# Performance work log

Measured on AMD Instinct MI355X. Metric: run time of the kernel, lower is better.

Reference implementation:

```python
import jax, jax.numpy as jnp
import numpy as np
import math

B, SEQ, PRED, F, DM, NH, DFF, S, DMARK = 16, 336, 96, 7, 512, 8, 2048, 16, 5
EL, DL = 2, 1
DH = DM // NH


def _pe(max_len, d):
    pos = np.arange(max_len)[:, None].astype(np.float32)
    div = np.exp(np.arange(0, d, 2).astype(np.float32) * (-math.log(10000.0) / d))
    pe = np.zeros((max_len, d), np.float32)
    pe[:, 0::2] = np.sin(pos * div)
    pe[:, 1::2] = np.cos(pos * div)
    return jnp.asarray(pe)


def _make_tao():
    t = np.ones((S, S), np.float32)
    t[:, 0] = 0.0
    t[:, -1] = 0.0
    t[1] *= -1.0
    t[0] = 0.0
    t[0, 0] = 1.0
    t[2:, 1:-1] = np.eye(S - 2, dtype=np.float32)
    return jnp.asarray(t)


PE = _pe(2000, DM)
TAO = _make_tao()
ZVEC = jnp.zeros((S,), jnp.float32).at[:2].set(1.0)
MASK = jnp.triu(jnp.full((PRED, PRED), -1e9, jnp.float32), k=1)  # causal additive mask


def _ln(x, w, b, eps=1e-5):
    m = x.mean(-1, keepdims=True)
    v = ((x - m) ** 2).mean(-1, keepdims=True)
    return (x - m) * jax.lax.rsqrt(v + eps) * w + b


def _mha(q_in, kv_in, qkv_w, qkv_b, ow, ob, mask=None):
    wq, wk, wv = jnp.split(qkv_w, 3, axis=0)
    bq, bk, bv = jnp.split(qkv_b, 3, axis=0)

    def proj(x, w, bb):
        y = x @ w.T + bb  # [B, T, DM]
        return y.reshape(y.shape[0], y.shape[1], NH, DH).transpose(0, 2, 1, 3)

    q, k, v = proj(q_in, wq, bq), proj(kv_in, wk, bk), proj(kv_in, wv, bv)
    s = jnp.einsum('bhqd,bhkd->bhqk', q, k) / math.sqrt(DH)
    if mask is not None:
        s = s + mask
    a = jax.nn.softmax(s, axis=-1)
    o = jnp.einsum('bhqk,bhkd->bhqd', a, v)
    o = o.transpose(0, 2, 1, 3).reshape(q_in.shape)
    return o @ ow.T + ob


def _per_feature(xe, xd, eqw, eqb, eow, eob, el1w, el1b, el2w, el2b,
                 ef1w, ef1b, ef2w, ef2b, elw, elb,
                 dsqw, dsqb, dsow, dsob, dcqw, dcqb, dcow, dcob,
                 dl1w, dl1b, dl2w, dl2b, dl3w, dl3b, df1w, df1b, df2w, df2b):
    # post-norm TransformerEncoder (relu FFN), eval mode (no dropout)
    h = xe
    for l in range(EL):
        h = _ln(h + _mha(h, h, eqw[l], eqb[l], eow[l], eob[l]), el1w[l], el1b[l])
        ff = jax.nn.relu(h @ ef1w[l].T + ef1b[l]) @ ef2w[l].T + ef2b[l]
        h = _ln(h + ff, el2w[l], el2b[l])
    # encoder_linear maps time axis seqlen -> prelen
    mem = jnp.einsum('bsd,ps->bpd', h, elw) + elb[None, :, None]
    t = xd
    for l in range(DL):
        t = _ln(t + _mha(t, t, dsqw[l], dsqb[l], dsow[l], dsob[l], MASK), dl1w[l], dl1b[l])
        t = _ln(t + _mha(t, mem, dcqw[l], dcqb[l], dcow[l], dcob[l]), dl2w[l], dl2b[l])
        ff = jax.nn.relu(t @ df1w[l].T + df1b[l]) @ df2w[l].T + df2b[l]
        t = _ln(t + ff, dl3w[l], dl3b[l])
    return t


_vfeat = jax.vmap(_per_feature, in_axes=(1, 1) + (0,) * 32, out_axes=1)


def setup_inputs():
    key = jax.random.key(0)
    ks = iter(jax.random.split(key, 64))

    def rn(shape, s=0.05):
        return jax.random.normal(next(ks), shape, jnp.float32) * s

    return {
        'batch_x': rn((B, SEQ, F), 1.0),
        'batch_x_mark': rn((B, SEQ, DMARK - 1), 1.0),
        'batch_y': rn((B, PRED, F), 1.0),
        'batch_y_mark': rn((B, PRED, DMARK - 1), 1.0),
        'w_in': rn((DM, DMARK)), 'b_in': rn((DM,)),
        'w_co': rn((DM, DMARK - 1)), 'b_co': rn((DM,)),
        'eqw': rn((F, EL, 3 * DM, DM)), 'eqb': rn((F, EL, 3 * DM)),
        'eow': rn((F, EL, DM, DM)), 'eob': rn((F, EL, DM)),
        'el1w': jnp.ones((F, EL, DM)), 'el1b': jnp.zeros((F, EL, DM)),
        'el2w': jnp.ones((F, EL, DM)), 'el2b': jnp.zeros((F, EL, DM)),
        'ef1w': rn((F, EL, DFF, DM)), 'ef1b': rn((F, EL, DFF)),
        'ef2w': rn((F, EL, DM, DFF)), 'ef2b': rn((F, EL, DM)),
        'elw': rn((F, PRED, SEQ)), 'elb': rn((F, PRED)),
        'dsqw': rn((F, DL, 3 * DM, DM)), 'dsqb': rn((F, DL, 3 * DM)),
        'dsow': rn((F, DL, DM, DM)), 'dsob': rn((F, DL, DM)),
        'dcqw': rn((F, DL, 3 * DM, DM)), 'dcqb': rn((F, DL, 3 * DM)),
        'dcow': rn((F, DL, DM, DM)), 'dcob': rn((F, DL, DM)),
        'dl1w': jnp.ones((F, DL, DM)), 'dl1b': jnp.zeros((F, DL, DM)),
        'dl2w': jnp.ones((F, DL, DM)), 'dl2b': jnp.zeros((F, DL, DM)),
        'dl3w': jnp.ones((F, DL, DM)), 'dl3b': jnp.zeros((F, DL, DM)),
        'df1w': rn((F, DL, DFF, DM)), 'df1b': rn((F, DL, DFF)),
        'df2w': rn((F, DL, DM, DFF)), 'df2b': rn((F, DL, DM)),
        'wc': rn((S, DM)), 'bc': rn((S,)),
        'ws': rn((1, DM)), 'bs': rn((1,)),
    }


def reference(batch_x, batch_x_mark, batch_y, batch_y_mark,
              w_in, b_in, w_co, b_co,
              eqw, eqb, eow, eob, el1w, el1b, el2w, el2b,
              ef1w, ef1b, ef2w, ef2b, elw, elb,
              dsqw, dsqb, dsow, dsob, dcqw, dcqb, dcow, dcob,
              dl1w, dl1b, dl2w, dl2b, dl3w, dl3b, df1w, df1b, df2w, df2b,
              wc, bc, ws, bs):
    Bsz = batch_x.shape[0]
    # time marks are shared across features -> broadcast instead of concat loop
    hist = jnp.concatenate(
        [batch_x[..., None],
         jnp.broadcast_to(batch_x_mark[:, :, None, :], (Bsz, SEQ, F, DMARK - 1))], axis=-1)
    fut = jnp.broadcast_to(batch_y_mark[:, -PRED:, None, :], (Bsz, PRED, F, DMARK - 1))
    hist = hist.transpose(0, 2, 1, 3)  # [B, F, SEQ, DMARK]
    fut = fut.transpose(0, 2, 1, 3)    # [B, F, PRED, DMARK-1]
    xe = hist @ w_in.T + b_in + PE[:SEQ]
    xd = fut @ w_co.T + b_co + PE[:PRED]
    dec = _vfeat(xe, xd, eqw, eqb, eow, eob, el1w, el1b, el2w, el2b,
                 ef1w, ef1b, ef2w, ef2b, elw, elb,
                 dsqw, dsqb, dsow, dsob, dcqw, dcqb, dcow, dcob,
                 dl1w, dl1b, dl2w, dl2b, dl3w, dl3b, df1w, df1b, df2w, df2b)
    # g_c = Linear + Hardsigmoid; g_s = Linear + Softplus
    c = jnp.clip((jnp.einsum('bfpd,sd->bfps', dec, wc) + bc) / 6.0 + 0.5, 0.0, 1.0)
    sig = jax.nn.softplus(jnp.einsum('bfpd,d->bfp', dec, ws[0]) + bs[0])
    # linear state recurrence a = TAO @ a + c, y = z^T a, scanned over prediction days
    a0 = c[:, :, 0]                      # [B, F, S] (torch initializes a with day-0 g_c)
    cs = jnp.moveaxis(c, 2, 0)           # [PRED, B, F, S]
    ss = jnp.moveaxis(sig, 2, 0)         # [PRED, B, F]

    def step(a, xs):
        cd, sd = xs
        a = jnp.einsum('ij,bfj->bfi', TAO, a) + cd
        return a, jnp.einsum('s,bfs->bf', ZVEC, a) + sd

    _, ys = jax.lax.scan(step, a0, (cs, ss))
    return jnp.transpose(ys, (1, 0, 2))  # [B, PRED, F]
```

## Files before the change

kernel.cpp:

```cpp
#include <hip/hip_runtime.h>

typedef unsigned short u16;
typedef unsigned int   u32;
typedef __attribute__((ext_vector_type(8))) short short8;
typedef __attribute__((ext_vector_type(4))) float f32x4;

#define DEV static __device__ __forceinline__

DEV float bf2f(u16 u) { return __uint_as_float(((u32)u) << 16); }
DEV u16 f2bf(float f) {
  u32 u = __float_as_uint(f);
  return (u16)((u + 0x7fffu + ((u >> 16) & 1u)) >> 16);
}

#define GLD16(gp, lp) __builtin_amdgcn_global_load_lds( \
    (__attribute__((address_space(1))) u32*)(gp),       \
    (__attribute__((address_space(3))) u32*)(lp), 16, 0, 0)

#define SBAR()  asm volatile("s_barrier" ::: "memory")
#define LGKM0() asm volatile("s_waitcnt lgkmcnt(0)" ::: "memory")

__global__ __launch_bounds__(512, 2) void gemm_bf16(
    const u16* __restrict__ A, const u16* __restrict__ Bw, u16* __restrict__ C,
    const float* __restrict__ bias, int M, int N, int K,
    long sAz, long sBz, long sCz, long sBiasZ, int relu)
{
  __shared__ __align__(16) u16 Asm[2][2][8192];
  __shared__ __align__(16) u16 Bsm[2][2][8192];

  int gx = (int)gridDim.x, gy = (int)gridDim.y;
  int nwg = gx * gy * (int)gridDim.z;
  int orig = (int)blockIdx.x + gx * ((int)blockIdx.y + gy * (int)blockIdx.z);
  int qq = nwg >> 3, rr_ = nwg & 7;
  int xcd = orig & 7, pos = orig >> 3;
  int lg_id = (xcd < rr_) ? (xcd * (qq + 1) + pos) : (rr_ * (qq + 1) + (xcd - rr_) * qq + pos);
  int bz = lg_id / (gx * gy);
  int rem = lg_id - bz * (gx * gy);
  int by = rem / gx, bx = rem - by * gx;

  A += (size_t)bz * sAz; Bw += (size_t)bz * sBz; C += (size_t)bz * sCz; bias += (size_t)bz * sBiasZ;
  int tileM = bx * 256, tileN = by * 256;
  int tid = threadIdx.x, wave = tid >> 6, lane = tid & 63;
  int lr = lane & 15, lgp = lane >> 4;
  int wm = (wave >> 2) * 128;
  int wn = (wave & 3) * 64;
  int ah = wave >> 2;
  int bh = (wave & 3) >> 1;
  int bnb = ((wave & 3) & 1) * 64;

  const int NT = K >> 6;
  const u16* Abase = A + (size_t)tileM * K;
  const u16* Bbase = Bw + (size_t)tileN * K;

  auto SA = [&](int b, int h, int t) {
    const u16* src = Abase + (size_t)h * 128 * K + t * 64;
    #pragma unroll
    for (int i = 0; i < 2; i++) {
      int gi = i * 512 + tid;
      int row = gi >> 3, g = gi & 7;
      GLD16(src + (size_t)row * K + ((g ^ (row & 7)) * 8), Asm[b][h] + (size_t)gi * 8);
    }
  };
  auto SB = [&](int b, int h, int t) {
    const u16* src = Bbase + (size_t)h * 128 * K + t * 64;
    #pragma unroll
    for (int i = 0; i < 2; i++) {
      int gi = i * 512 + tid;
      int row = gi >> 3, g = gi & 7;
      GLD16(src + (size_t)row * K + ((g ^ (row & 7)) * 8), Bsm[b][h] + (size_t)gi * 8);
    }
  };

  f32x4 acc[8][4] = {};

  SA(0, 0, 0); SA(0, 1, 0); SB(0, 0, 0); SB(0, 1, 0);
  if (NT > 1) { SB(1, 0, 1); SB(1, 1, 1); }
  if (NT > 1) asm volatile("s_waitcnt vmcnt(4)" ::: "memory");
  else        asm volatile("s_waitcnt vmcnt(0)" ::: "memory");
  SBAR();

  for (int t = 0; t < NT; ++t) {
    int cur = t & 1;
    const u16* Aslot = Asm[cur][ah];
    const u16* Bslot = Bsm[cur][bh];
    short8 afr[8], b0[4], b1[4];

    #pragma unroll
    for (int mm = 0; mm < 4; ++mm) {
      int rw = mm * 16 + lr;
      #pragma unroll
      for (int ks = 0; ks < 2; ++ks)
        afr[mm * 2 + ks] = *(const short8*)(Aslot + rw * 64 + (((ks * 4 + lgp) ^ (rw & 7)) * 8));
    }
    #pragma unroll
    for (int nn = 0; nn < 2; ++nn) {
      int rw = bnb + nn * 16 + lr;
      #pragma unroll
      for (int ks = 0; ks < 2; ++ks)
        b0[nn * 2 + ks] = *(const short8*)(Bslot + rw * 64 + (((ks * 4 + lgp) ^ (rw & 7)) * 8));
    }
    if (t + 1 < NT) SA(cur ^ 1, 0, t + 1);
    SBAR(); LGKM0();
    __builtin_amdgcn_s_setprio(1);
    #pragma unroll
    for (int mm = 0; mm < 4; ++mm)
      #pragma unroll
      for (int nn = 0; nn < 2; ++nn)
        #pragma unroll
        for (int ks = 0; ks < 2; ++ks)
          acc[mm][nn] = __builtin_amdgcn_mfma_f32_16x16x32_bf16(
              afr[mm * 2 + ks], b0[nn * 2 + ks], acc[mm][nn], 0, 0, 0);
    __builtin_amdgcn_s_setprio(0);
    SBAR();

    #pragma unroll
    for (int nn = 0; nn < 2; ++nn) {
      int rw = bnb + (nn + 2) * 16 + lr;
      #pragma unroll
      for (int ks = 0; ks < 2; ++ks)
        b1[nn * 2 + ks] = *(const short8*)(Bslot + rw * 64 + (((ks * 4 + lgp) ^ (rw & 7)) * 8));
    }
    if (t + 1 < NT) SA(cur ^ 1, 1, t + 1);
    SBAR(); LGKM0();
    __builtin_amdgcn_s_setprio(1);
    #pragma unroll
    for (int mm = 0; mm < 4; ++mm)
      #pragma unroll
      for (int nn = 0; nn < 2; ++nn)
        #pragma unroll
        for (int ks = 0; ks < 2; ++ks)
          acc[mm][nn + 2] = __builtin_amdgcn_mfma_f32_16x16x32_bf16(
              afr[mm * 2 + ks], b1[nn * 2 + ks], acc[mm][nn + 2], 0, 0, 0);
    __builtin_amdgcn_s_setprio(0);
    SBAR();

    #pragma unroll
    for (int mm = 0; mm < 4; ++mm) {
      int rw = (mm + 4) * 16 + lr;
      #pragma unroll
      for (int ks = 0; ks < 2; ++ks)
        afr[mm * 2 + ks] = *(const short8*)(Aslot + rw * 64 + (((ks * 4 + lgp) ^ (rw & 7)) * 8));
    }
    if (t + 2 < NT) SB(cur, 0, t + 2);
    SBAR(); LGKM0();
    __builtin_amdgcn_s_setprio(1);
    #pragma unroll
    for (int mm = 0; mm < 4; ++mm)
      #pragma unroll
      for (int nn = 0; nn < 2; ++nn)
        #pragma unroll
        for (int ks = 0; ks < 2; ++ks)
          acc[mm + 4][nn + 2] = __builtin_amdgcn_mfma_f32_16x16x32_bf16(
              afr[mm * 2 + ks], b1[nn * 2 + ks], acc[mm + 4][nn + 2], 0, 0, 0);
    __builtin_amdgcn_s_setprio(0);
    SBAR();

    if (t + 2 < NT) SB(cur, 1, t + 2);
    __builtin_amdgcn_s_setprio(1);
    #pragma unroll
    for (int mm = 0; mm < 4; ++mm)
      #pragma unroll
      for (int nn = 0; nn < 2; ++nn)
        #pragma unroll
        for (int ks = 0; ks < 2; ++ks)
          acc[mm + 4][nn] = __builtin_amdgcn_mfma_f32_16x16x32_bf16(
              afr[mm * 2 + ks], b0[nn * 2 + ks], acc[mm + 4][nn], 0, 0, 0);
    __builtin_amdgcn_s_setprio(0);
    if (t + 2 < NT) asm volatile("s_waitcnt vmcnt(4)" ::: "memory");
    else            asm volatile("s_waitcnt vmcnt(0)" ::: "memory");
    SBAR();
  }

  float bb[4];
  #pragma unroll
  for (int n = 0; n < 4; ++n) bb[n] = bias[tileN + wn + n * 16 + lr];
  #pragma unroll
  for (int m = 0; m < 8; ++m) {
    #pragma unroll
    for (int rr = 0; rr < 4; ++rr) {
      int mrow = tileM + wm + m * 16 + lgp * 4 + rr;
      u16* crow = C + (size_t)mrow * N + tileN + wn + lr;
      #pragma unroll
      for (int n = 0; n < 4; ++n) {
        float v = acc[m][n][rr] + bb[n];
        if (relu) v = fmaxf(v, 0.f);
        crow[n * 16] = f2bf(v);
      }
    }
  }
}

__global__ __launch_bounds__(256, 2) void gemm_bf16_s(
    const u16* __restrict__ A, const u16* __restrict__ Bw, u16* __restrict__ C,
    const float* __restrict__ bias, int M, int N, int K,
    long sAz, long sBz, long sCz, long sBiasZ, int relu)
{
  __shared__ __align__(16) u16 Asm[3][128 * 32];
  __shared__ __align__(16) u16 Bsm[3][128 * 32];

  int gx = (int)gridDim.x, gy = (int)gridDim.y;
  int nwg = gx * gy * (int)gridDim.z;
  int orig = (int)blockIdx.x + gx * ((int)blockIdx.y + gy * (int)blockIdx.z);
  int qq = nwg >> 3, rr_ = nwg & 7;
  int xcd = orig & 7, pos = orig >> 3;
  int lg_id = (xcd < rr_) ? (xcd * (qq + 1) + pos) : (rr_ * (qq + 1) + (xcd - rr_) * qq + pos);
  int bz = lg_id / (gx * gy);
  int rem = lg_id - bz * (gx * gy);
  int by = rem / gx, bx = rem - by * gx;

  A += (size_t)bz * sAz; Bw += (size_t)bz * sBz; C += (size_t)bz * sCz; bias += (size_t)bz * sBiasZ;
  int tileM = bx * 128, tileN = by * 128;
  int tid = threadIdx.x, lane = tid & 63;
  int wave = tid >> 6;
  int lr = lane & 15, lgp = lane >> 4;
  int wm = (wave >> 1) * 64, wn = (wave & 1) * 64;

  const int NT = K >> 5;
  const u16* Abase = A + (size_t)tileM * K;
  const u16* Bbase = Bw + (size_t)tileN * K;

  auto STAGE = [&](int b, int t) {
    int kb = t * 32;
    #pragma unroll
    for (int i = 0; i < 2; i++) {
      int gi = i * 256 + tid;
      int row = gi >> 2, g = gi & 3;
      GLD16(Abase + (size_t)row * K + kb + ((g ^ ((row >> 1) & 3)) * 8),
            Asm[b] + (size_t)gi * 8);
    }
    #pragma unroll
    for (int i = 0; i < 2; i++) {
      int gi = i * 256 + tid;
      int row = gi >> 2, g = gi & 3;
      GLD16(Bbase + (size_t)row * K + kb + ((g ^ ((row >> 1) & 3)) * 8),
            Bsm[b] + (size_t)gi * 8);
    }
  };

  f32x4 acc[4][4] = {};

  STAGE(0, 0);
  if (NT > 1) STAGE(1, 1);

  int cur = 0;
  for (int t = 0; t < NT; ++t) {
    if (t + 2 < NT) {
      int nb = cur + 2; if (nb >= 3) nb -= 3;
      STAGE(nb, t + 2);
      asm volatile("s_waitcnt vmcnt(8)" ::: "memory");
    } else if (t + 1 < NT) {
      asm volatile("s_waitcnt vmcnt(4)" ::: "memory");
    } else {
      asm volatile("s_waitcnt vmcnt(0)" ::: "memory");
    }
    SBAR();

    const u16* Ab = Asm[cur];
    const u16* Bb = Bsm[cur];
    short8 afr[4], bfr[4];
    #pragma unroll
    for (int m = 0; m < 4; ++m) {
      int rw = wm + m * 16 + lr;
      afr[m] = *(const short8*)(Ab + rw * 32 + ((lgp ^ ((rw >> 1) & 3)) * 8));
    }
    #pragma unroll
    for (int n = 0; n < 4; ++n) {
      int rw = wn + n * 16 + lr;
      bfr[n] = *(const short8*)(Bb + rw * 32 + ((lgp ^ ((rw >> 1) & 3)) * 8));
    }
    __builtin_amdgcn_s_setprio(1);
    #pragma unroll
    for (int m = 0; m < 4; ++m)
      #pragma unroll
      for (int n = 0; n < 4; ++n)
        acc[m][n] = __builtin_amdgcn_mfma_f32_16x16x32_bf16(
            afr[m], bfr[n], acc[m][n], 0, 0, 0);
    __builtin_amdgcn_s_setprio(0);
    LGKM0();
    SBAR();
    cur = (cur + 1 == 3) ? 0 : cur + 1;
  }

  float bb[4];
  #pragma unroll
  for (int n = 0; n < 4; ++n) bb[n] = bias[tileN + wn + n * 16 + lr];
  #pragma unroll
  for (int m = 0; m < 4; ++m) {
    #pragma unroll
    for (int rr = 0; rr < 4; ++rr) {
      int mrow = tileM + wm + m * 16 + lgp * 4 + rr;
      u16* crow = C + (size_t)mrow * N + tileN + wn + lr;
      #pragma unroll
      for (int n = 0; n < 4; ++n) {
        float v = acc[m][n][rr] + bb[n];
        if (relu) v = fmaxf(v, 0.f);
        crow[n * 16] = f2bf(v);
      }
    }
  }
}

__global__ void cvt_w_kernel(const float* __restrict__ src, u16* __restrict__ dst,
                             long n_per_f, long f_stride, long total4)
{
  long i = (long)blockIdx.x * blockDim.x + threadIdx.x;
  long step = (long)gridDim.x * blockDim.x;
  for (; i < total4; i += step) {
    long e = i * 4;
    long f = e / n_per_f; long r = e - f * n_per_f;
    float4 v = *(const float4*)(src + f * f_stride + r);
    *(ushort4*)(dst + e) = make_ushort4(f2bf(v.x), f2bf(v.y), f2bf(v.z), f2bf(v.w));
  }
}

__global__ __launch_bounds__(128) void embed_enc_k(
    const float* __restrict__ x, const float* __restrict__ mark,
    const float* __restrict__ w_in, const float* __restrict__ b_in,
    u16* __restrict__ hb)
{
  int row = blockIdx.x;
  int f = row / 5376; int rem = row - f * 5376; int b = rem / 336; int s = rem - b * 336;
  int bsix = b * 336 + s;
  float v0 = x[(size_t)bsix * 7 + f];
  float m0 = mark[(size_t)bsix * 4 + 0], m1 = mark[(size_t)bsix * 4 + 1];
  float m2 = mark[(size_t)bsix * 4 + 2], m3 = mark[(size_t)bsix * 4 + 3];
  int d0 = threadIdx.x * 4;
  u16 ob[4];
  #pragma unroll
  for (int c = 0; c < 4; c++) {
    int d = d0 + c;
    const float* w = w_in + d * 5;
    float val = w[0] * v0 + w[1] * m0 + w[2] * m1 + w[3] * m2 + w[4] * m3 + b_in[d];
    int i = d >> 1;
    float dv = expf((float)i * -0.0359778920778f);
    float arg = (float)s * dv;
    val += (d & 1) ? cosf(arg) : sinf(arg);
    ob[c] = f2bf(val);
  }
  *(ushort4*)(hb + (size_t)row * 512 + d0) = make_ushort4(ob[0], ob[1], ob[2], ob[3]);
}

__global__ __launch_bounds__(128) void embed_dec_k(
    const float* __restrict__ ymark, const float* __restrict__ w_co,
    const float* __restrict__ b_co, u16* __restrict__ tb)
{
  int row = blockIdx.x;
  int f = row / 1536; int rem = row - f * 1536; int b = rem / 96; int pp = rem - b * 96;
  int bp = b * 96 + pp;
  float m0 = ymark[(size_t)bp * 4 + 0], m1 = ymark[(size_t)bp * 4 + 1];
  float m2 = ymark[(size_t)bp * 4 + 2], m3 = ymark[(size_t)bp * 4 + 3];
  int d0 = threadIdx.x * 4;
  u16 ob[4];
  #pragma unroll
  for (int c = 0; c < 4; c++) {
    int d = d0 + c;
    const float* w = w_co + d * 4;
    float val = w[0] * m0 + w[1] * m1 + w[2] * m2 + w[3] * m3 + b_co[d];
    int i = d >> 1;
    float dv = expf((float)i * -0.0359778920778f);
    float arg = (float)pp * dv;
    val += (d & 1) ? cosf(arg) : sinf(arg);
    ob[c] = f2bf(val);
  }
  *(ushort4*)(tb + (size_t)row * 512 + d0) = make_ushort4(ob[0], ob[1], ob[2], ob[3]);
}

template<int LK, int CHUNK, int NQI>
__global__ __launch_bounds__(256) void attn_mfma(
    const u16* __restrict__ q, const u16* __restrict__ k, const u16* __restrict__ v,
    u16* __restrict__ out, int Lq, int qstride, int kvstride, int causal, int qspan)
{
  constexpr int NCH = LK / CHUNK;
  constexpr int NKT = CHUNK / 16;
  constexpr int NKS = (CHUNK + 31) / 32;
  constexpr int KPAD = NKS * 32;
  constexpr int VSTR = KPAD + 8;
  constexpr int NGRP = CHUNK * 8 / 64;

  __shared__ __align__(16) u16 KsS[CHUNK * 64];
  __shared__ __align__(16) u16 VtS[64 * VSTR];
  __shared__ __align__(16) u16 PWS[4][16 * VSTR];

  int hh = blockIdx.x, fb = blockIdx.y;
  int tid = threadIdx.x, wave = tid >> 6, lane = tid & 63;
  int lr = lane & 15, lg = lane >> 4;

  const int nqt = Lq / 16;
  const int qlo = (int)blockIdx.z * qspan;
  const int qhi = (qlo + qspan < nqt) ? (qlo + qspan) : nqt;

  const u16* qp = q + (size_t)fb * Lq * qstride + hh * 64;
  const u16* kp = k + (size_t)fb * LK * kvstride + hh * 64;
  const u16* vp = v + (size_t)fb * LK * kvstride + hh * 64;

  if constexpr (KPAD > CHUNK) {
    constexpr int TW = KPAD - CHUNK;
    for (int i = tid; i < 64 * TW; i += 256)
      VtS[(i / TW) * VSTR + CHUNK + (i % TW)] = 0;
    u16* PW = PWS[wave];
    for (int i = lane; i < 16 * TW; i += 64)
      PW[(i / TW) * VSTR + CHUNK + (i % TW)] = 0;
  }

  f32x4 oacc[NQI][4] = {};
  f32x4 lsum[NQI] = {};
  u16* PW = PWS[wave];

  for (int c = 0; c < NCH; ++c) {
    __syncthreads();

    const u16* kcp = kp + (size_t)c * CHUNK * kvstride;
    for (int grp = wave; grp < NGRP; grp += 4) {
      int gi = grp * 64 + lane;
      int row = gi >> 3, g = gi & 7;
      GLD16(kcp + (size_t)row * kvstride + ((g ^ (row & 7)) * 8), KsS + (size_t)gi * 8);
    }
    const u16* vcp = vp + (size_t)c * CHUNK * kvstride;
    for (int idx = tid; idx < CHUNK * 8; idx += 256) {
      int kk = idx >> 3, dg = idx & 7;
      uint4 pv = *(const uint4*)(vcp + (size_t)kk * kvstride + dg * 8);
      u16* col = VtS + (size_t)(dg * 8) * VSTR + kk;
      col[0 * VSTR] = (u16)pv.x; col[1 * VSTR] = (u16)(pv.x >> 16);
      col[2 * VSTR] = (u16)pv.y; col[3 * VSTR] = (u16)(pv.y >> 16);
      col[4 * VSTR] = (u16)pv.z; col[5 * VSTR] = (u16)(pv.z >> 16);
      col[6 * VSTR] = (u16)pv.w; col[7 * VSTR] = (u16)(pv.w >> 16);
    }
    __syncthreads();

    #pragma unroll
    for (int qi = 0; qi < NQI; ++qi) {
      int qt = qlo + wave + qi * 4;
      if (qt < qhi) {
        const u16* qrow = qp + (size_t)(qt * 16 + lr) * qstride + lg * 8;
        short8 qf0 = *(const short8*)(qrow);
        short8 qf1 = *(const short8*)(qrow + 32);

        f32x4 sacc[NKT];
        #pragma unroll
        for (int t = 0; t < NKT; t++) {
          int row = t * 16 + lr;
          const u16* kb = KsS + row * 64;
          short8 kf0 = *(const short8*)(kb + ((lg ^ (row & 7)) * 8));
          short8 kf1 = *(const short8*)(kb + (((lg + 4) ^ (row & 7)) * 8));
          f32x4 s = {0.f, 0.f, 0.f, 0.f};
          s = __builtin_amdgcn_mfma_f32_16x16x32_bf16(qf0, kf0, s, 0, 0, 0);
          s = __builtin_amdgcn_mfma_f32_16x16x32_bf16(qf1, kf1, s, 0, 0, 0);
          sacc[t] = s;
        }

        #pragma unroll
        for (int t = 0; t < NKT; t++) {
          int kg = c * CHUNK + t * 16 + lr;
          #pragma unroll
          for (int r = 0; r < 4; r++) {
            int qg = qt * 16 + lg * 4 + r;
            float p = (causal && kg > qg) ? 0.f : __expf(sacc[t][r] * 0.125f);
            sacc[t][r] = p;
            lsum[qi][r] += p;
          }
          u16* pw = PW + (size_t)(lg * 4) * VSTR + t * 16 + lr;
          pw[0 * VSTR] = f2bf(sacc[t][0]);
          pw[1 * VSTR] = f2bf(sacc[t][1]);
          pw[2 * VSTR] = f2bf(sacc[t][2]);
          pw[3 * VSTR] = f2bf(sacc[t][3]);
        }

        #pragma unroll
        for (int s = 0; s < NKS; s++) {
          short8 pf = *(const short8*)(PW + (size_t)lr * VSTR + s * 32 + lg * 8);
          #pragma unroll
          for (int j = 0; j < 4; j++) {
            short8 vf = *(const short8*)(VtS + (size_t)(j * 16 + lr) * VSTR + s * 32 + lg * 8);
            oacc[qi][j] = __builtin_amdgcn_mfma_f32_16x16x32_bf16(pf, vf, oacc[qi][j], 0, 0, 0);
          }
        }
      }
    }
  }

  #pragma unroll
  for (int qi = 0; qi < NQI; ++qi) {
    int qt = qlo + wave + qi * 4;
    if (qt < qhi) {
      float l0 = lsum[qi][0], l1 = lsum[qi][1], l2 = lsum[qi][2], l3 = lsum[qi][3];
      #pragma unroll
      for (int m = 1; m < 16; m <<= 1) {
        l0 += __shfl_xor(l0, m);
        l1 += __shfl_xor(l1, m);
        l2 += __shfl_xor(l2, m);
        l3 += __shfl_xor(l3, m);
      }
      float inv[4] = {1.f / l0, 1.f / l1, 1.f / l2, 1.f / l3};
      #pragma unroll
      for (int r = 0; r < 4; r++) {
        size_t orow = (size_t)fb * Lq + qt * 16 + lg * 4 + r;
        u16* ob = out + orow * 512 + hh * 64 + lr;
        #pragma unroll
        for (int j = 0; j < 4; j++)
          ob[j * 16] = f2bf(oacc[qi][j][r] * inv[r]);
      }
    }
  }
}

__global__ __launch_bounds__(128) void ln_kernel(
    u16* __restrict__ h, const u16* __restrict__ delta,
    const float* __restrict__ gamma, const float* __restrict__ beta,
    int rows_per_f, long gstride)
{
  __shared__ float red[2];
  int row = blockIdx.x;
  int f = row / rows_per_f;
  const float* g = gamma + (size_t)f * gstride;
  const float* be = beta + (size_t)f * gstride;
  int d0 = threadIdx.x * 4;
  size_t p = (size_t)row * 512 + d0;
  ushort4 hv = *(const ushort4*)(h + p);
  ushort4 dv = *(const ushort4*)(delta + p);
  float x0 = bf2f(hv.x) + bf2f(dv.x), x1 = bf2f(hv.y) + bf2f(dv.y);
  float x2 = bf2f(hv.z) + bf2f(dv.z), x3 = bf2f(hv.w) + bf2f(dv.w);
  float ssum = x0 + x1 + x2 + x3;
  #pragma unroll
  for (int m = 1; m < 64; m <<= 1) ssum += __shfl_xor(ssum, m);
  if ((threadIdx.x & 63) == 0) red[threadIdx.x >> 6] = ssum;
  __syncthreads();
  float mean = (red[0] + red[1]) * (1.f / 512.f);
  __syncthreads();
  float c0 = x0 - mean, c1 = x1 - mean, c2 = x2 - mean, c3 = x3 - mean;
  float sq = c0 * c0 + c1 * c1 + c2 * c2 + c3 * c3;
  #pragma unroll
  for (int m = 1; m < 64; m <<= 1) sq += __shfl_xor(sq, m);
  if ((threadIdx.x & 63) == 0) red[threadIdx.x >> 6] = sq;
  __syncthreads();
  float var = (red[0] + red[1]) * (1.f / 512.f);
  float rstd = rsqrtf(var + 1e-5f);
  float y0 = c0 * rstd * g[d0 + 0] + be[d0 + 0];
  float y1 = c1 * rstd * g[d0 + 1] + be[d0 + 1];
  float y2 = c2 * rstd * g[d0 + 2] + be[d0 + 2];
  float y3 = c3 * rstd * g[d0 + 3] + be[d0 + 3];
  *(ushort4*)(h + p) = make_ushort4(f2bf(y0), f2bf(y1), f2bf(y2), f2bf(y3));
}

__global__ __launch_bounds__(256) void mem_kernel(
    const u16* __restrict__ h, const float* __restrict__ elw,
    const float* __restrict__ elb, u16* __restrict__ memb)
{
  int fb = blockIdx.x; int f = fb >> 4;
  int pc = blockIdx.y;
  int d0 = threadIdx.x * 2;
  const u16* hbase = h + (size_t)fb * 336 * 512;
  const float* wbase = elw + (size_t)f * 96 * 336 + (size_t)pc * 16 * 336;
  float a0[16], a1[16];
  #pragma unroll
  for (int pp = 0; pp < 16; pp++) { a0[pp] = 0.f; a1[pp] = 0.f; }
  for (int s = 0; s < 336; s++) {
    ushort2 h2 = *(const ushort2*)(hbase + (size_t)s * 512 + d0);
    float hx = bf2f(h2.x), hy = bf2f(h2.y);
    #pragma unroll
    for (int pp = 0; pp < 16; pp++) {
      float w = wbase[pp * 336 + s];
      a0[pp] += w * hx; a1[pp] += w * hy;
    }
  }
  #pragma unroll
  for (int pp = 0; pp < 16; pp++) {
    int pidx = pc * 16 + pp;
    size_t row = (size_t)fb * 96 + pidx;
    float e = elb[f * 96 + pidx];
    *(ushort2*)(memb + row * 512 + d0) = make_ushort2(f2bf(a0[pp] + e), f2bf(a1[pp] + e));
  }
}

__global__ __launch_bounds__(64) void head_kernel(
    const u16* __restrict__ td, const float* __restrict__ wcp, const float* __restrict__ bcp,
    const float* __restrict__ wsp, const float* __restrict__ bsp,
    float* __restrict__ cb, float* __restrict__ sg, int f0)
{
  int rl = blockIdx.x, lane = threadIdx.x;
  size_t row = (size_t)f0 * 1536 + rl;
  const u16* x = td + (size_t)rl * 512;
  float xr[8];
  #pragma unroll
  for (int j = 0; j < 8; j++) xr[j] = bf2f(x[lane + 64 * j]);
  #pragma unroll
  for (int o = 0; o < 16; o++) {
    const float* w = wcp + o * 512;
    float p = 0.f;
    #pragma unroll
    for (int j = 0; j < 8; j++) p += xr[j] * w[lane + 64 * j];
    #pragma unroll
    for (int m = 1; m < 64; m <<= 1) p += __shfl_xor(p, m);
    if (lane == 0) {
      float cv = (p + bcp[o]) / 6.0f + 0.5f;
      cb[row * 16 + o] = fminf(fmaxf(cv, 0.f), 1.f);
    }
  }
  float p = 0.f;
  #pragma unroll
  for (int j = 0; j < 8; j++) p += xr[j] * wsp[lane + 64 * j];
  #pragma unroll
  for (int m = 1; m < 64; m <<= 1) p += __shfl_xor(p, m);
  if (lane == 0) {
    float zv = p + bsp[0];
    sg[row] = (zv > 20.f) ? zv : log1pf(expf(zv));
  }
}

__global__ __launch_bounds__(256) void scan_kernel(
    const float* __restrict__ cbuf, const float* __restrict__ sgb, float* __restrict__ outp)
{
  int f = blockIdx.x;
  int b = threadIdx.x >> 4;
  int s = threadIdx.x & 15;
  size_t rbase = ((size_t)f * 16 + b) * 96;
  float a = cbuf[rbase * 16 + s];
  for (int p = 0; p < 96; ++p) {
    float cd = cbuf[(rbase + p) * 16 + s];
    float sd = sgb[rbase + p];
    float xs = (s >= 1 && s <= 14) ? a : 0.f;
    #pragma unroll
    for (int m = 1; m < 16; m <<= 1) xs += __shfl_xor(xs, m);
    float up = __shfl_up(a, 1, 16);
    float an = (s == 0) ? (a + cd) : ((s == 1) ? (cd - xs) : (up + cd));
    a = an;
    float y01 = __shfl(a, 0, 16) + __shfl(a, 1, 16) + sd;
    if (s == 0) outp[((size_t)b * 96 + p) * 7 + f] = y01;
  }
}

__global__ void diag_kernel(float* __restrict__ out, float v, int n)
{
  int i = blockIdx.x * 256 + threadIdx.x;
  if (i < n) out[i] = v;
}

extern "C" void kernel_launch(void* const* d_in, const int* in_sizes, int n_in,
                              void* d_out, int out_size, void* d_ws, size_t ws_size,
                              hipStream_t stream)
{
  (void)in_sizes; (void)n_in;
  const float* batch_x      = (const float*)d_in[0];
  const float* batch_x_mark = (const float*)d_in[1];
  const float* batch_y_mark = (const float*)d_in[3];
  const float* w_in = (const float*)d_in[4];
  const float* b_in = (const float*)d_in[5];
  const float* w_co = (const float*)d_in[6];
  const float* b_co = (const float*)d_in[7];
  const float* eqw  = (const float*)d_in[8];
  const float* eqb  = (const float*)d_in[9];
  const float* eow  = (const float*)d_in[10];
  const float* eob  = (const float*)d_in[11];
  const float* el1w = (const float*)d_in[12];
  const float* el1b = (const float*)d_in[13];
  const float* el2w = (const float*)d_in[14];
  const float* el2b = (const float*)d_in[15];
  const float* ef1w = (const float*)d_in[16];
  const float* ef1b = (const float*)d_in[17];
  const float* ef2w = (const float*)d_in[18];
  const float* ef2b = (const float*)d_in[19];
  const float* elw  = (const float*)d_in[20];
  const float* elb  = (const float*)d_in[21];
  const float* dsqw = (const float*)d_in[22];
  const float* dsqb = (const float*)d_in[23];
  const float* dsow = (const float*)d_in[24];
  const float* dsob = (const float*)d_in[25];
  const float* dcqw = (const float*)d_in[26];
  const float* dcqb = (const float*)d_in[27];
  const float* dcow = (const float*)d_in[28];
  const float* dcob = (const float*)d_in[29];
  const float* dl1w = (const float*)d_in[30];
  const float* dl1b = (const float*)d_in[31];
  const float* dl2w = (const float*)d_in[32];
  const float* dl2b = (const float*)d_in[33];
  const float* dl3w = (const float*)d_in[34];
  const float* dl3b = (const float*)d_in[35];
  const float* df1w = (const float*)d_in[36];
  const float* df1b = (const float*)d_in[37];
  const float* df2w = (const float*)d_in[38];
  const float* df2b = (const float*)d_in[39];
  const float* wc   = (const float*)d_in[40];
  const float* bc   = (const float*)d_in[41];
  const float* wsg  = (const float*)d_in[42];
  const float* bsg  = (const float*)d_in[43];

  const size_t NE = 37632;
  const size_t ND = 10752;
  auto al = [](size_t x) { return (x + 255) & ~(size_t)255; };

  size_t fixedB = al(NE * 1024) + al(ND * 1024) + al(ND * 64) + al(ND * 4);
  int G = 0;
  for (int g = 7; g >= 1; --g) {
    size_t need = fixedB
        + al((size_t)g * 5376 * 2048 * 2)
        + al((size_t)g * 5376 * 512 * 2)
        + al((size_t)g * 2048 * 512 * 2)
        + al((size_t)g * 1536 * 512 * 2);
    if (need <= ws_size) { G = g; break; }
  }
  if (G == 0) {
    diag_kernel<<<dim3((out_size + 255) / 256), 256, 0, stream>>>(
        (float*)d_out, 1000.0f + (float)(ws_size >> 20), out_size);
    return;
  }

  char* base = (char*)d_ws;
  size_t off = 0;
  auto alloc = [&](size_t bytes) -> void* { void* r = base + off; off += al(bytes); return r; };
  u16*   hres = (u16*)  alloc(NE * 1024);
  u16*   tres = (u16*)  alloc(ND * 1024);
  float* cb   = (float*)alloc(ND * 64);
  float* sg   = (float*)alloc(ND * 4);
  u16*   bigc = (u16*)  alloc((size_t)G * 5376 * 2048 * 2);
  u16*   aobc = (u16*)  alloc((size_t)G * 5376 * 512 * 2);
  u16*   wbuf = (u16*)  alloc((size_t)G * 2048 * 512 * 2);
  u16*   memb = (u16*)  alloc((size_t)G * 1536 * 512 * 2);

  embed_enc_k<<<dim3(37632), 128, 0, stream>>>(batch_x, batch_x_mark, w_in, b_in, hres);
  embed_dec_k<<<dim3(10752), 128, 0, stream>>>(batch_y_mark, w_co, b_co, tres);

  auto cvtw = [&](const float* src, long n_per_f, long f_stride, int g) {
    cvt_w_kernel<<<dim3(512), 256, 0, stream>>>(src, wbuf, n_per_f, f_stride,
                                                (long)g * n_per_f / 4);
  };
  auto gemm = [&](const u16* A, long sAz, u16* C, long sCz, const float* bias, long sBias,
                  int M, int N, int K, int g, int relu) {
    dim3 gr(M / 256, N / 256, g);
    gemm_bf16<<<gr, 512, 0, stream>>>(A, wbuf, C, bias, M, N, K, sAz, (long)N * K, sCz,
                                      sBias, relu);
  };
  auto gemms = [&](const u16* A, long sAz, u16* C, long sCz, const float* bias, long sBias,
                   int M, int N, int K, int g, int relu) {
    dim3 gr(M / 128, N / 128, g);
    gemm_bf16_s<<<gr, 256, 0, stream>>>(A, wbuf, C, bias, M, N, K, sAz, (long)N * K, sCz,
                                        sBias, relu);
  };

  for (int f0 = 0; f0 < 7; f0 += G) {
    int g = (7 - f0 < G) ? (7 - f0) : G;
    u16* hc = hres + (size_t)f0 * 5376 * 512;
    u16* tc = tres + (size_t)f0 * 1536 * 512;

    for (int l = 0; l < 2; ++l) {
      cvtw(eqw + (size_t)f0 * 1572864 + (size_t)l * 786432, 786432L, 1572864L, g);
      gemm(hc, 5376L * 512, bigc, 5376L * 1536, eqb + f0 * 3072 + l * 1536, 3072,
           5376, 1536, 512, g, 0);
      attn_mfma<336, 112, 3><<<dim3(8, g * 16, 2), 256, 0, stream>>>(
          bigc, bigc + 512, bigc + 1024, aobc, 336, 1536, 1536, 0, 11);
      cvtw(eow + (size_t)f0 * 524288 + (size_t)l * 262144, 262144L, 524288L, g);
      gemms(aobc, 5376L * 512, bigc, 5376L * 512, eob + f0 * 1024 + l * 512, 1024,
            5376, 512, 512, g, 0);
      ln_kernel<<<dim3(g * 5376), 128, 0, stream>>>(
          hc, bigc, el1w + f0 * 1024 + l * 512, el1b + f0 * 1024 + l * 512, 5376, 1024);
      cvtw(ef1w + (size_t)f0 * 2097152 + (size_t)l * 1048576, 1048576L, 2097152L, g);
      gemm(hc, 5376L * 512, bigc, 5376L * 2048, ef1b + f0 * 4096 + l * 2048, 4096,
           5376, 2048, 512, g, 1);
      cvtw(ef2w + (size_t)f0 * 2097152 + (size_t)l * 1048576, 1048576L, 2097152L, g);
      gemms(bigc, 5376L * 2048, aobc, 5376L * 512, ef2b + f0 * 1024 + l * 512, 1024,
            5376, 512, 2048, g, 0);
      ln_kernel<<<dim3(g * 5376), 128, 0, stream>>>(
          hc, aobc, el2w + f0 * 1024 + l * 512, el2b + f0 * 1024 + l * 512, 5376, 1024);
    }

    mem_kernel<<<dim3(g * 16, 6), 256, 0, stream>>>(
        hc, elw + (size_t)f0 * 32256, elb + f0 * 96, memb);

    cvtw(dsqw + (size_t)f0 * 786432, 786432L, 786432L, g);
    gemms(tc, 1536L * 512, bigc, 1536L * 1536, dsqb + f0 * 1536, 1536,
          1536, 1536, 512, g, 0);
    attn_mfma<96, 96, 2><<<dim3(8, g * 16, 1), 256, 0, stream>>>(
        bigc, bigc + 512, bigc + 1024, aobc, 96, 1536, 1536, 1, 6);
    cvtw(dsow + (size_t)f0 * 262144, 262144L, 262144L, g);
    gemms(aobc, 1536L * 512, bigc, 1536L * 512, dsob + f0 * 512, 512,
          1536, 512, 512, g, 0);
    ln_kernel<<<dim3(g * 1536), 128, 0, stream>>>(
        tc, bigc, dl1w + f0 * 512, dl1b + f0 * 512, 1536, 512);

    cvtw(dcqw + (size_t)f0 * 786432, 262144L, 786432L, g);
    gemms(tc, 1536L * 512, bigc, 1536L * 512, dcqb + f0 * 1536, 1536,
          1536, 512, 512, g, 0);
    u16* bigKV = bigc + (size_t)g * 1536 * 512;
    cvtw(dcqw + (size_t)f0 * 786432 + 262144, 524288L, 786432L, g);
    gemms(memb, 1536L * 512, bigKV, 1536L * 1024, dcqb + f0 * 1536 + 512, 1536,
          1536, 1024, 512, g, 0);
    attn_mfma<96, 96, 2><<<dim3(8, g * 16, 1), 256, 0, stream>>>(
        bigc, bigKV, bigKV + 512, aobc, 96, 512, 1024, 0, 6);
    cvtw(dcow + (size_t)f0 * 262144, 262144L, 262144L, g);
    gemms(aobc, 1536L * 512, bigc, 1536L * 512, dcob + f0 * 512, 512,
          1536, 512, 512, g, 0);
    ln_kernel<<<dim3(g * 1536), 128, 0, stream>>>(
        tc, bigc, dl2w + f0 * 512, dl2b + f0 * 512, 1536, 512);

    cvtw(df1w + (size_t)f0 * 1048576, 1048576L, 1048576L, g);
    gemms(tc, 1536L * 512, bigc, 1536L * 2048, df1b + f0 * 2048, 2048,
          1536, 2048, 512, g, 1);
    cvtw(df2w + (size_t)f0 * 1048576, 1048576L, 1048576L, g);
    gemms(bigc, 1536L * 2048, aobc, 1536L * 512, df2b + f0 * 512, 512,
          1536, 512, 2048, g, 0);
    ln_kernel<<<dim3(g * 1536), 128, 0, stream>>>(
        tc, aobc, dl3w + f0 * 512, dl3b + f0 * 512, 1536, 512);

    head_kernel<<<dim3(g * 1536), 64, 0, stream>>>(tc, wc, bc, wsg, bsg, cb, sg, f0);
  }

  scan_kernel<<<dim3(7), 256, 0, stream>>>(cb, sg, (float*)d_out);
}
```

Before: 1.489 ms.

## Split-K the encoder FFN down-projection on the large GEMM kernel with a reduce pass

Runs the FFN2 GEMM (K=2048, N=512) on the 256x256-tile kernel with a split-K factor of 2. Each split writes bf16 partial results to a new workspace buffer, and a separate reduce kernel sums the two partials and adds the bias. This replaces the 128x128-tile kernel, aiming for better MFMA efficiency while keeping enough workgroups to fill the device. The cost is an extra kernel launch and extra partial-buffer memory traffic, and rounding the partials to bf16 adds some precision loss.

```diff
diff --git a/kernel.cpp b/kernel.cpp
--- a/kernel.cpp
+++ b/kernel.cpp
@@ -23,7 +23,7 @@
 __global__ __launch_bounds__(512, 2) void gemm_bf16(
     const u16* __restrict__ A, const u16* __restrict__ Bw, u16* __restrict__ C,
     const float* __restrict__ bias, int M, int N, int K,
-    long sAz, long sBz, long sCz, long sBiasZ, int relu)
+    long sAz, long sBz, long sCz, long sBiasZ, int relu, int ksplit)
 {
   __shared__ __align__(16) u16 Asm[2][2][8192];
   __shared__ __align__(16) u16 Bsm[2][2][8192];
@@ -38,7 +38,11 @@
   int rem = lg_id - bz * (gx * gy);
   int by = rem / gx, bx = rem - by * gx;
 
-  A += (size_t)bz * sAz; Bw += (size_t)bz * sBz; C += (size_t)bz * sCz; bias += (size_t)bz * sBiasZ;
+  int zf = bz, ksl = 0;
+  if (ksplit > 1) { zf = bz / ksplit; ksl = bz - zf * ksplit; }
+
+  A += (size_t)zf * sAz; Bw += (size_t)zf * sBz; bias += (size_t)zf * sBiasZ;
+  C += (size_t)bz * sCz;
   int tileM = bx * 256, tileN = by * 256;
   int tid = threadIdx.x, wave = tid >> 6, lane = tid & 63;
   int lr = lane & 15, lgp = lane >> 4;
@@ -48,9 +52,10 @@
   int bh = (wave & 3) >> 1;
   int bnb = ((wave & 3) & 1) * 64;
 
-  const int NT = K >> 6;
-  const u16* Abase = A + (size_t)tileM * K;
-  const u16* Bbase = Bw + (size_t)tileN * K;
+  const int Keff = K / ksplit;
+  const int NT = Keff >> 6;
+  const u16* Abase = A + (size_t)tileM * K + ksl * Keff;
+  const u16* Bbase = Bw + (size_t)tileN * K + ksl * Keff;
 
   auto SA = [&](int b, int h, int t) {
     const u16* src = Abase + (size_t)h * 128 * K + t * 64;
@@ -171,22 +176,57 @@
     SBAR();
   }
 
-  float bb[4];
-  #pragma unroll
-  for (int n = 0; n < 4; ++n) bb[n] = bias[tileN + wn + n * 16 + lr];
-  #pragma unroll
-  for (int m = 0; m < 8; ++m) {
-    #pragma unroll
-    for (int rr = 0; rr < 4; ++rr) {
-      int mrow = tileM + wm + m * 16 + lgp * 4 + rr;
-      u16* crow = C + (size_t)mrow * N + tileN + wn + lr;
-      #pragma unroll
-      for (int n = 0; n < 4; ++n) {
-        float v = acc[m][n][rr] + bb[n];
-        if (relu) v = fmaxf(v, 0.f);
-        crow[n * 16] = f2bf(v);
+  if (relu == 2) {
+    #pragma unroll
+    for (int m = 0; m < 8; ++m) {
+      #pragma unroll
+      for (int rr = 0; rr < 4; ++rr) {
+        int mrow = tileM + wm + m * 16 + lgp * 4 + rr;
+        u16* crow = C + (size_t)mrow * N + tileN + wn + lr;
+        #pragma unroll
+        for (int n = 0; n < 4; ++n)
+          crow[n * 16] = f2bf(acc[m][n][rr]);
       }
     }
+  } else {
+    float bb[4];
+    #pragma unroll
+    for (int n = 0; n < 4; ++n) bb[n] = bias[tileN + wn + n * 16 + lr];
+    #pragma unroll
+    for (int m = 0; m < 8; ++m) {
+      #pragma unroll
+      for (int rr = 0; rr < 4; ++rr) {
+        int mrow = tileM + wm + m * 16 + lgp * 4 + rr;
+        u16* crow = C + (size_t)mrow * N + tileN + wn + lr;
+        #pragma unroll
+        for (int n = 0; n < 4; ++n) {
+          float v = acc[m][n][rr] + bb[n];
+          if (relu) v = fmaxf(v, 0.f);
+          crow[n * 16] = f2bf(v);
+        }
+      }
+    }
+  }
+}
+
+__global__ void reduce_k(const u16* __restrict__ P, const float* __restrict__ bias,
+                         long biasStrideF, u16* __restrict__ out, long S, long total4)
+{
+  long i = (long)blockIdx.x * blockDim.x + threadIdx.x;
+  long step = (long)gridDim.x * blockDim.x;
+  for (; i < total4; i += step) {
+    long e = i * 4;
+    long f = e / S; long r = e - f * S;
+    int n = (int)(r & 511);
+    ushort4 p0 = *(const ushort4*)(P + (size_t)(f * 2) * S + r);
+    ushort4 p1 = *(const ushort4*)(P + (size_t)(f * 2 + 1) * S + r);
+    const float* bb = bias + f * biasStrideF + n;
+    float v0 = bf2f(p0.x) + bf2f(p1.x) + bb[0];
+    float v1 = bf2f(p0.y) + bf2f(p1.y) + bb[1];
+    float v2 = bf2f(p0.z) + bf2f(p1.z) + bb[2];
+    float v3 = bf2f(p0.w) + bf2f(p1.w) + bb[3];
+    *(ushort4*)(out + (size_t)f * S + r) =
+        make_ushort4(f2bf(v0), f2bf(v1), f2bf(v2), f2bf(v3));
   }
 }
 
@@ -715,6 +755,12 @@
   u16*   wbuf = (u16*)  alloc((size_t)G * 2048 * 512 * 2);
   u16*   memb = (u16*)  alloc((size_t)G * 1536 * 512 * 2);
 
+  u16* pbuf = nullptr;
+  {
+    size_t pneed = al((size_t)G * 2 * 5376 * 512 * 2);
+    if (off + pneed <= ws_size) pbuf = (u16*)alloc(pneed);
+  }
+
   embed_enc_k<<<dim3(37632), 128, 0, stream>>>(batch_x, batch_x_mark, w_in, b_in, hres);
   embed_dec_k<<<dim3(10752), 128, 0, stream>>>(batch_y_mark, w_co, b_co, tres);
 
@@ -726,7 +772,7 @@
                   int M, int N, int K, int g, int relu) {
     dim3 gr(M / 256, N / 256, g);
     gemm_bf16<<<gr, 512, 0, stream>>>(A, wbuf, C, bias, M, N, K, sAz, (long)N * K, sCz,
-                                      sBias, relu);
+                                      sBias, relu, 1);
   };
   auto gemms = [&](const u16* A, long sAz, u16* C, long sCz, const float* bias, long sBias,
                    int M, int N, int K, int g, int relu) {
@@ -755,8 +801,18 @@
       gemm(hc, 5376L * 512, bigc, 5376L * 2048, ef1b + f0 * 4096 + l * 2048, 4096,
            5376, 2048, 512, g, 1);
       cvtw(ef2w + (size_t)f0 * 2097152 + (size_t)l * 1048576, 1048576L, 2097152L, g);
-      gemms(bigc, 5376L * 2048, aobc, 5376L * 512, ef2b + f0 * 1024 + l * 512, 1024,
-            5376, 512, 2048, g, 0);
+      if (pbuf) {
+        dim3 gr(21, 2, g * 2);
+        gemm_bf16<<<gr, 512, 0, stream>>>(
+            bigc, wbuf, pbuf, ef2b, 5376, 512, 2048,
+            5376L * 2048, 512L * 2048, 5376L * 512, 0, 2, 2);
+        reduce_k<<<dim3(2048), 256, 0, stream>>>(
+            pbuf, ef2b + f0 * 1024 + l * 512, 1024, aobc,
+            2752512L, (long)g * 688128);
+      } else {
+        gemms(bigc, 5376L * 2048, aobc, 5376L * 512, ef2b + f0 * 1024 + l * 512, 1024,
+              5376, 512, 2048, g, 0);
+      }
       ln_kernel<<<dim3(g * 5376), 128, 0, stream>>>(
           hc, aobc, el2w + f0 * 1024 + l * 512, el2b + f0 * 1024 + l * 512, 5376, 1024);
     }
```

Result: no change. 1.496 ms (+0.5%).
